# Kernel optimization log

Hardware: AMD Instinct MI355X
Metric: run time of the kernel (lower is better)

## Reference

```python
import jax, jax.numpy as jnp
import numpy as np

# --- LIF neuron (spikingjelly LIFNode, single-step, tau=2.0, hard reset, ATan surrogate) ---
# With zero initial membrane potential, one step gives h = x / tau, spike = heaviside(h - v_th).
ALPHA = 2.0  # ATan surrogate default alpha
TAU = 2.0    # LIFNode default tau
V_TH = 1.0

@jax.custom_vjp
def atan_heaviside(x):
    return (x >= 0.0).astype(x.dtype)

def _ah_fwd(x):
    return (x >= 0.0).astype(x.dtype), x

def _ah_bwd(res, g):
    # d/dx of ATan surrogate: alpha / (2 * (1 + (pi/2 * alpha * x)^2))
    return (g * (ALPHA / (2.0 * (1.0 + (jnp.pi / 2.0 * ALPHA * res) ** 2))),)

atan_heaviside.defvjp(_ah_fwd, _ah_bwd)

def lif(x):
    return atan_heaviside(x / TAU - V_TH)

DIM, NUM_HEADS, TOPK = 256, 8, 4
WT, WH, WW = 2, 4, 4

def setup_inputs() -> dict:
    key = jax.random.key(0)
    k1, k2, k3, k4, k5 = jax.random.split(key, 5)
    T, B, Lt, Lh, Lw, C = 4, 2, 8, 32, 32, DIM
    x = jax.random.normal(k1, (T, B, Lt, Lh, Lw, C), dtype=jnp.float32)
    w_qkv = jax.random.normal(k2, (C, 3 * C), dtype=jnp.float32) * 0.02
    b_qkv = jax.random.normal(k3, (3 * C,), dtype=jnp.float32) * 0.02
    w_proj = jax.random.normal(k4, (C, C), dtype=jnp.float32) * 0.02
    b_proj = jax.random.normal(k5, (C,), dtype=jnp.float32) * 0.02
    return {"x": x, "w_qkv": w_qkv, "b_qkv": b_qkv, "w_proj": w_proj, "b_proj": b_proj}

def reference(x, w_qkv, b_qkv, w_proj, b_proj):
    T, B, Lt, Lh, Lw, C = x.shape
    H = NUM_HEADS
    D = C // H
    scale = D ** -0.5
    lt, lh, lw = Lt // WT, Lh // WH, Lw // WW
    W = WT * WH * WW          # num_wins = 32
    S = lt * lh * lw          # win_size = 256

    # window partition: [T,B,Lt,Lh,Lw,C] -> [T,B,W,S,C]
    xw = x.reshape(T, B, WT, lt, WH, lh, WW, lw, C)
    xw = xw.transpose(0, 1, 2, 4, 6, 3, 5, 7, 8).reshape(T, B, W, S, C)

    # region routing: mean over timesteps and tokens -> [B,W,C]
    region = xw.mean(axis=(0, 3))
    scores = jnp.einsum('bwc,bvc->bwv', region, region) * scale  # [B,W,W]
    idx = jax.lax.top_k(scores, TOPK)[1]                          # [B,W,K] int32

    # qkv projection + spiking activations
    qkv = xw @ w_qkv + b_qkv                                      # [T,B,W,S,3C]
    q, k, v = jnp.split(qkv, 3, axis=-1)
    q, k, v = lif(q), lif(k), lif(v)
    q = q.reshape(T, B, W, S, H, D)
    k = k.reshape(T, B, W, S, H, D)
    v = v.reshape(T, B, W, S, H, D)

    # gather routed KV blocks: k_g[t,b,w,j] = k[t,b,idx[b,w,j]]
    b_ix = jnp.arange(B)[:, None, None]
    k_g = k[:, b_ix, idx].reshape(T, B, W, TOPK * S, H, D)        # [T,B,W,K*S,H,D]
    v_g = v[:, b_ix, idx].reshape(T, B, W, TOPK * S, H, D)

    # linear attention: kv = k^T v, out = q @ kv, normalized by q @ sum(k)
    kv = jnp.einsum('tbwnhd,tbwnhe->tbwhde', k_g, v_g)            # [T,B,W,H,D,D]
    out = jnp.einsum('tbwshd,tbwhde->tbwshe', q, kv)              # [T,B,W,S,H,D]
    den = jnp.einsum('tbwshd,tbwhd->tbwsh', q, k_g.sum(axis=3))[..., None]
    out = out / (den + 1e-6)

    out = out.reshape(T, B, W, S, C) @ w_proj + b_proj

    # window reverse: [T,B,W,S,C] -> [T,B,Lt,Lh,Lw,C]
    out = out.reshape(T, B, WT, WH, WW, lt, lh, lw, C)
    out = out.transpose(0, 1, 2, 5, 3, 6, 4, 7, 8).reshape(T, B, Lt, Lh, Lw, C)
    return out
```

## Files before the change

### kernel.cpp

```cpp
#include <hip/hip_runtime.h>
#include <hip/hip_bf16.h>
#include <stdint.h>

#define NT 4
#define NB 2
#define NW 32
#define NS 256
#define NC 256
#define NH 8
#define ND 32
#define NK 4

typedef unsigned int u32;
typedef unsigned long long u64;
typedef unsigned short u16;
typedef __attribute__((ext_vector_type(8))) short bf16x8;
typedef __attribute__((ext_vector_type(4))) float f32x4;

__device__ __forceinline__ int wofs(int w) {
  return (w >> 4) * 4096 + ((w >> 2) & 3) * 256 + (w & 3) * 8;
}
__device__ __forceinline__ int sofs(int s) {
  return ((s >> 6) << 10) + (((s >> 3) & 7) << 5) + (s & 7);
}
__device__ __forceinline__ size_t x_off(int t, int b, int w, int s, int c) {
  return ((size_t)((t * NB + b) * 8192 + wofs(w) + sofs(s))) * NC + c;
}

__device__ __forceinline__ u32 f2bf(float f) {
  union { float f; u32 i; } u; u.f = f;
  return (u.i + 0x7FFFu + ((u.i >> 16) & 1u)) >> 16;
}

__device__ __forceinline__ void gload16(const u16* g, u16* l) {
  __builtin_amdgcn_global_load_lds(
      (const __attribute__((address_space(1))) void*)g,
      (__attribute__((address_space(3))) void*)l, 16, 0, 0);
}

__global__ __launch_bounds__(256) void k_prep(const float* __restrict__ x,
                                              const float* __restrict__ w_qkv,
                                              u16* __restrict__ xw,
                                              u16* __restrict__ bt,
                                              float* __restrict__ region) {
  int blk = blockIdx.x, tid = threadIdx.x;
  if (blk >= 512) {
    int n = (blk - 512) * 8 + (tid >> 5);
    int kc = tid & 31;
    u16 vals[8];
#pragma unroll
    for (int j = 0; j < 8; ++j)
      vals[j] = (u16)f2bf(w_qkv[(size_t)(kc * 8 + j) * 768 + n]);
    *reinterpret_cast<uint4*>(&bt[(size_t)n * 256 + kc * 8]) =
        *reinterpret_cast<const uint4*>(vals);
    return;
  }
  __shared__ float sums[4][4][NC];
  int g = tid >> 6, c4 = tid & 63;
  size_t base = (size_t)blk * 128;
  float4 s[4];
#pragma unroll
  for (int ww = 0; ww < 4; ++ww) s[ww] = make_float4(0.f, 0.f, 0.f, 0.f);
#pragma unroll
  for (int p = 0; p < 32; ++p) {
    int row = p * 4 + g;
    float4 v = *reinterpret_cast<const float4*>(&x[(base + row) * NC + c4 * 4]);
    uint2 bf;
    bf.x = f2bf(v.x) | (f2bf(v.y) << 16);
    bf.y = f2bf(v.z) | (f2bf(v.w) << 16);
    *reinterpret_cast<uint2*>(&xw[(base + row) * NC + c4 * 4]) = bf;
    int ww = (p & 7) >> 1;
    s[ww].x += v.x; s[ww].y += v.y; s[ww].z += v.z; s[ww].w += v.w;
  }
#pragma unroll
  for (int ww = 0; ww < 4; ++ww)
    *reinterpret_cast<float4*>(&sums[ww][g][c4 * 4]) = s[ww];
  __syncthreads();
  int b = (blk >> 6) & 1;
  int wt = ((blk >> 3) & 7) >> 2, wh = (blk & 7) >> 1;
  int v0 = wt * 16 + wh * 4;
  int c = tid;
#pragma unroll
  for (int ww = 0; ww < 4; ++ww) {
    float tot = (sums[ww][0][c] + sums[ww][1][c] + sums[ww][2][c] + sums[ww][3][c]) *
                (1.0f / 1024.0f);
    atomicAdd(&region[((size_t)b * NW + v0 + ww) * NC + c], tot);
  }
}

__global__ __launch_bounds__(256) void k_scores(const float* __restrict__ region,
                                                int* __restrict__ idx) {
  __shared__ float rs[NW][NC];
  __shared__ float scval[NW];
  int blk = blockIdx.x;
  int b = blk >> 5, w = blk & 31;
  int tid = threadIdx.x;
  for (int i = tid; i < NW * NC; i += 256)
    rs[i >> 8][i & 255] = region[(size_t)b * NW * NC + i];
  __syncthreads();
  int v = tid >> 3, l8 = tid & 7;
  float sum = 0.f;
  const float* a = rs[w];
  const float* bb = rs[v];
#pragma unroll
  for (int j = 0; j < 32; ++j) sum += a[l8 * 32 + j] * bb[l8 * 32 + j];
  sum += __shfl_xor(sum, 1);
  sum += __shfl_xor(sum, 2);
  sum += __shfl_xor(sum, 4);
  if (l8 == 0) scval[v] = sum * 0.17677669529663687f;
  __syncthreads();
  if (tid == 0) {
    float sc[NW];
#pragma unroll
    for (int j = 0; j < NW; ++j) sc[j] = scval[j];
    for (int kk = 0; kk < NK; ++kk) {
      float best = -__builtin_inff(); int bi = 0;
      for (int j = 0; j < NW; ++j)
        if (sc[j] > best) { best = sc[j]; bi = j; }
      idx[(b * NW + w) * NK + kk] = bi;
      sc[bi] = -__builtin_inff();
    }
  }
}

__global__ __launch_bounds__(256) void k_gemm(const u16* __restrict__ xw,
                                              const u16* __restrict__ bt,
                                              const float* __restrict__ b_qkv,
                                              u32* __restrict__ qb, u32* __restrict__ kb,
                                              u32* __restrict__ vb,
                                              u32* __restrict__ winflag) {
  __shared__ __align__(16) u16 As[2][128 * 32];
  __shared__ __align__(16) u16 Bs[2][128 * 32];
  __shared__ u32 wfl;

  const int tid = threadIdx.x;
  const int v = (blockIdx.x & 7) * 384 + (blockIdx.x >> 3);
  const int mt = v / 6, nt = v % 6;
  const int m0 = mt * 128, n0 = nt * 128;
  const int wave = tid >> 6, lane = tid & 63;
  const int wr = wave >> 1, wc = wave & 1;

  if (tid == 0) wfl = 0;

  const f32x4 vz = {0.f, 0.f, 0.f, 0.f};
  f32x4 acc[4][4];
#pragma unroll
  for (int m = 0; m < 4; ++m)
#pragma unroll
    for (int n = 0; n < 4; ++n) acc[m][n] = vz;

  auto stage = [&](int buf, int ks) {
    const int k0 = ks * 32;
#pragma unroll
    for (int p = 0; p < 2; ++p) {
      int idx2 = p * 256 + wave * 64 + lane;
      int row = idx2 >> 2, sl = idx2 & 3;
      int ssl = sl ^ ((row >> 1) & 3);
      int lbase = (p * 256 + wave * 64) * 8;
      gload16(&xw[(size_t)(m0 + row) * 256 + k0 + ssl * 8], &As[buf][lbase]);
      gload16(&bt[(size_t)(n0 + row) * 256 + k0 + ssl * 8], &Bs[buf][lbase]);
    }
  };

  stage(0, 0);
  __syncthreads();
#pragma unroll
  for (int ks = 0; ks < 8; ++ks) {
    const int buf = ks & 1;
    if (ks < 7) stage(buf ^ 1, ks + 1);
    bf16x8 afr[4], bfr[4];
#pragma unroll
    for (int m = 0; m < 4; ++m) {
      int r = wr * 64 + m * 16 + (lane & 15);
      int phys = (lane >> 4) ^ ((r >> 1) & 3);
      afr[m] = *reinterpret_cast<const bf16x8*>(&As[buf][r * 32 + phys * 8]);
    }
#pragma unroll
    for (int n = 0; n < 4; ++n) {
      int r = wc * 64 + n * 16 + (lane & 15);
      int phys = (lane >> 4) ^ ((r >> 1) & 3);
      bfr[n] = *reinterpret_cast<const bf16x8*>(&Bs[buf][r * 32 + phys * 8]);
    }
#pragma unroll
    for (int m = 0; m < 4; ++m)
#pragma unroll
      for (int n = 0; n < 4; ++n)
        acc[m][n] = __builtin_amdgcn_mfma_f32_16x16x32_bf16(afr[m], bfr[n], acc[m][n], 0, 0, 0);
    __syncthreads();
  }

  float bias[4];
#pragma unroll
  for (int n = 0; n < 4; ++n) bias[n] = b_qkv[n0 + wc * 64 + n * 16 + (lane & 15)];
  u32* dst = (nt < 2) ? qb : (nt < 4) ? kb : vb;
  const int h0 = (nt * 4) & 7;
  const int g = lane >> 4;
  u32 wfl_loc = 0;
#pragma unroll
  for (int m = 0; m < 4; ++m)
#pragma unroll
    for (int r = 0; r < 4; ++r) {
      u32 words[2];
#pragma unroll
      for (int np = 0; np < 2; ++np) {
        u64 b0 = __ballot(acc[m][2 * np][r] + bias[2 * np] >= 2.0f);
        u64 b1 = __ballot(acc[m][2 * np + 1][r] + bias[2 * np + 1] >= 2.0f);
        words[np] = (u32)((b0 >> (g * 16)) & 0xFFFFu) |
                    ((u32)((b1 >> (g * 16)) & 0xFFFFu) << 16);
      }
      if ((lane & 15) < 2) {
        int np = lane & 1;
        int row = wr * 64 + m * 16 + g * 4 + r;
        u32 wv = words[np];
        dst[(size_t)(m0 + row) * NH + h0 + wc * 2 + np] = wv;
        if (wv) wfl_loc |= 1u << ((row & 31) >> 3);
      }
    }
  if (wfl_loc) atomicOr(&wfl, wfl_loc);
  __syncthreads();
  if (tid == 0 && wfl) {
    int t = mt >> 7, b = (mt >> 6) & 1, Lt = (mt >> 3) & 7, hh = mt & 7;
    int w0 = (Lt >> 2) * 16 + (hh >> 1) * 4;
    u32 bit = (nt < 2) ? 1u : (nt < 4) ? 2u : 4u;
    for (int ww = 0; ww < 4; ++ww)
      if (wfl & (1u << ww))
        atomicOr(&winflag[(t * NB + b) * NW + w0 + ww], bit);
  }
}

__global__ __launch_bounds__(256) void k_attn(const u32* __restrict__ qb,
                                              const u32* __restrict__ kb,
                                              const u32* __restrict__ vb,
                                              const int* __restrict__ idx,
                                              const u32* __restrict__ winflag,
                                              const float* __restrict__ w_proj,
                                              const float* __restrict__ b_proj,
                                              float* __restrict__ out) {
  __shared__ u32 qs[64 * NH];
  __shared__ unsigned short kvc[NH * ND * ND];
  __shared__ u32 ksum[NH * ND];
  __shared__ float attnrow[NC];

  int blk = blockIdx.x;
  int wid = blk >> 2, sc = blk & 3;
  int t = wid >> 6, b = (wid >> 5) & 1, w = wid & 31;
  int s0 = sc * 64;
  int tid = threadIdx.x;

  u32 fs = winflag[(t * NB + b) * NW + w];
  int wj[NK];
  u32 fk = 0, fv = 0;
#pragma unroll
  for (int j = 0; j < NK; ++j) {
    wj[j] = idx[(b * NW + w) * NK + j];
    u32 f = winflag[(t * NB + b) * NW + wj[j]];
    fk |= f & 2u; fv |= f & 4u;
  }
  bool skip = !(fs & 1u) || !fk || !fv;

  if (skip) {
    float bp = b_proj[tid];
    for (int s = s0; s < s0 + 64; ++s) out[x_off(t, b, w, s, tid)] = bp;
    return;
  }

  int tb = (t * NB + b) * 8192;
  size_t gb[NK];
#pragma unroll
  for (int j = 0; j < NK; ++j) gb[j] = (size_t)(tb + wofs(wj[j])) * NH;
  size_t qbase = (size_t)(tb + wofs(w)) * NH;
  for (int i = tid; i < 64 * NH; i += 256)
    qs[i] = qb[qbase + (size_t)sofs(s0 + (i >> 3)) * NH + (i & 7)];
  {
    int h = tid >> 5, d = tid & 31;
    u32 cnt = 0;
    for (int n = 0; n < NK * NS; ++n)
      cnt += (kb[gb[n >> 8] + (size_t)sofs(n & 255) * NH + h] >> d) & 1u;
    ksum[tid] = cnt;
  }
  for (int p = tid; p < NH * ND * ND; p += 256) {
    int h = p >> 10, d = (p >> 5) & 31, e = p & 31;
    u32 cnt = 0;
    for (int n = 0; n < NK * NS; ++n) {
      size_t a = gb[n >> 8] + (size_t)sofs(n & 255) * NH + h;
      cnt += ((kb[a] >> d) & (vb[a] >> e)) & 1u;
    }
    kvc[p] = (unsigned short)cnt;
  }
  __syncthreads();
  int h = tid >> 5, e = tid & 31;
  float bpv = b_proj[tid];
  for (int sl = 0; sl < 64; ++sl) {
    u32 qw = qs[sl * NH + h];
    float num = 0.f, den = 0.f;
    for (int d = 0; d < ND; ++d) {
      if ((qw >> d) & 1u) {
        den += (float)ksum[h * ND + d];
        num += (float)kvc[h * ND * ND + d * ND + e];
      }
    }
    attnrow[tid] = num / (den + 1e-6f);
    __syncthreads();
    float acc = bpv;
    for (int c = 0; c < NC; ++c) acc += attnrow[c] * w_proj[c * NC + tid];
    out[x_off(t, b, w, s0 + sl, tid)] = acc;
    __syncthreads();
  }
}

extern "C" void kernel_launch(void* const* d_in, const int* in_sizes, int n_in,
                              void* d_out, int out_size, void* d_ws, size_t ws_size,
                              hipStream_t stream) {
  const float* x      = (const float*)d_in[0];
  const float* w_qkv  = (const float*)d_in[1];
  const float* b_qkv  = (const float*)d_in[2];
  const float* w_proj = (const float*)d_in[3];
  const float* b_proj = (const float*)d_in[4];
  float* out = (float*)d_out;

  char* ws = (char*)d_ws;
  int* idx       = (int*)(ws + 0x200000);
  u16* bt        = (u16*)(ws + 0x201000);
  u32* winflag   = (u32*)(ws + 0x270000);
  float* region  = (float*)(ws + 0x271000);
  u32* qb        = (u32*)(ws + 0x300000);
  u32* kb        = qb + (size_t)NT * NB * NW * NS * NH;
  u32* vb        = kb + (size_t)NT * NB * NW * NS * NH;
  u16* xw        = (u16*)(ws + 0x900000);

  hipMemsetAsync(ws + 0x270000, 0, 0x11000, stream);
  k_prep<<<608, 256, 0, stream>>>(x, w_qkv, xw, bt, region);
  k_scores<<<NB * NW, 256, 0, stream>>>(region, idx);
  k_gemm<<<3072, 256, 0, stream>>>(xw, bt, b_qkv, qb, kb, vb, winflag);
  k_attn<<<NT * NB * NW * 4, 256, 0, stream>>>(qb, kb, vb, idx, winflag, w_proj, b_proj, out);
}
```

Measured before the change: 88.07 us.

## Enlarge QKV GEMM tiles to 256x256 with 512 threads and explicit waitcnt pipelining

The QKV projection GEMM moves from 128x128 tiles with K-step 32 and 256 threads to 256x256 tiles with K-step 64, 512 threads, and 8x4 MFMA accumulators per wave. Double buffering now relies on explicit vmcnt waits and raw s_barrier with sched_barriers, so the next tile's loads overlap compute. The goal is more data reuse per LDS load, fewer blocks, and fewer barriers. The cost is much more LDS (128KB per block) and more accumulator registers, which limits occupancy to about one block per CU. The winflag and head-index logic is re-derived for the new tile mapping.

```diff
diff --git a/kernel.cpp b/kernel.cpp
--- a/kernel.cpp
+++ b/kernel.cpp
@@ -123,108 +123,127 @@
   }
 }
 
-__global__ __launch_bounds__(256) void k_gemm(const u16* __restrict__ xw,
-                                              const u16* __restrict__ bt,
-                                              const float* __restrict__ b_qkv,
-                                              u32* __restrict__ qb, u32* __restrict__ kb,
-                                              u32* __restrict__ vb,
-                                              u32* __restrict__ winflag) {
-  __shared__ __align__(16) u16 As[2][128 * 32];
-  __shared__ __align__(16) u16 Bs[2][128 * 32];
+__global__ __launch_bounds__(512, 2) void k_gemm(const u16* __restrict__ xw,
+                                                 const u16* __restrict__ bt,
+                                                 const float* __restrict__ b_qkv,
+                                                 u32* __restrict__ qb, u32* __restrict__ kb,
+                                                 u32* __restrict__ vb,
+                                                 u32* __restrict__ winflag) {
+  __shared__ __align__(16) u16 As[2][256 * 64];
+  __shared__ __align__(16) u16 Bs[2][256 * 64];
   __shared__ u32 wfl;
 
   const int tid = threadIdx.x;
-  const int v = (blockIdx.x & 7) * 384 + (blockIdx.x >> 3);
-  const int mt = v / 6, nt = v % 6;
-  const int m0 = mt * 128, n0 = nt * 128;
+  const int v = (blockIdx.x & 7) * 96 + (blockIdx.x >> 3);
+  const int mt = v / 3, nt = v % 3;
+  const int m0 = mt * 256, n0 = nt * 256;
   const int wave = tid >> 6, lane = tid & 63;
-  const int wr = wave >> 1, wc = wave & 1;
+  const int wr = wave >> 2, wc = wave & 3;
 
   if (tid == 0) wfl = 0;
 
   const f32x4 vz = {0.f, 0.f, 0.f, 0.f};
-  f32x4 acc[4][4];
-#pragma unroll
-  for (int m = 0; m < 4; ++m)
+  f32x4 acc[8][4];
+#pragma unroll
+  for (int m = 0; m < 8; ++m)
 #pragma unroll
     for (int n = 0; n < 4; ++n) acc[m][n] = vz;
 
-  auto stage = [&](int buf, int ks) {
-    const int k0 = ks * 32;
-#pragma unroll
-    for (int p = 0; p < 2; ++p) {
-      int idx2 = p * 256 + wave * 64 + lane;
-      int row = idx2 >> 2, sl = idx2 & 3;
-      int ssl = sl ^ ((row >> 1) & 3);
-      int lbase = (p * 256 + wave * 64) * 8;
-      gload16(&xw[(size_t)(m0 + row) * 256 + k0 + ssl * 8], &As[buf][lbase]);
-      gload16(&bt[(size_t)(n0 + row) * 256 + k0 + ssl * 8], &Bs[buf][lbase]);
+  auto stage = [&](int buf, int kt) {
+    const int k0 = kt * 64;
+#pragma unroll
+    for (int i = 0; i < 4; ++i) {
+      int c = i * 512 + tid;
+      int row = c >> 3, p = c & 7;
+      int sl = p ^ (row & 7);
+      gload16(&xw[(size_t)(m0 + row) * 256 + k0 + sl * 8],
+              &As[buf][(i * 512 + wave * 64) * 8]);
+    }
+#pragma unroll
+    for (int i = 0; i < 4; ++i) {
+      int c = i * 512 + tid;
+      int row = c >> 3, p = c & 7;
+      int sl = p ^ (row & 7);
+      gload16(&bt[(size_t)(n0 + row) * 256 + k0 + sl * 8],
+              &Bs[buf][(i * 512 + wave * 64) * 8]);
     }
   };
 
   stage(0, 0);
-  __syncthreads();
-#pragma unroll
-  for (int ks = 0; ks < 8; ++ks) {
-    const int buf = ks & 1;
-    if (ks < 7) stage(buf ^ 1, ks + 1);
-    bf16x8 afr[4], bfr[4];
-#pragma unroll
-    for (int m = 0; m < 4; ++m) {
-      int r = wr * 64 + m * 16 + (lane & 15);
-      int phys = (lane >> 4) ^ ((r >> 1) & 3);
-      afr[m] = *reinterpret_cast<const bf16x8*>(&As[buf][r * 32 + phys * 8]);
-    }
-#pragma unroll
-    for (int n = 0; n < 4; ++n) {
-      int r = wc * 64 + n * 16 + (lane & 15);
-      int phys = (lane >> 4) ^ ((r >> 1) & 3);
-      bfr[n] = *reinterpret_cast<const bf16x8*>(&Bs[buf][r * 32 + phys * 8]);
-    }
-#pragma unroll
-    for (int m = 0; m < 4; ++m)
-#pragma unroll
-      for (int n = 0; n < 4; ++n)
-        acc[m][n] = __builtin_amdgcn_mfma_f32_16x16x32_bf16(afr[m], bfr[n], acc[m][n], 0, 0, 0);
-    __syncthreads();
+#pragma unroll
+  for (int kt = 0; kt < 4; ++kt) {
+    const int buf = kt & 1;
+    if (kt < 3) {
+      stage(buf ^ 1, kt + 1);
+      __builtin_amdgcn_sched_barrier(0);
+      asm volatile("s_waitcnt vmcnt(8)" ::: "memory");
+    } else {
+      __builtin_amdgcn_sched_barrier(0);
+      asm volatile("s_waitcnt vmcnt(0)" ::: "memory");
+    }
+    __builtin_amdgcn_s_barrier();
+    __builtin_amdgcn_sched_barrier(0);
+#pragma unroll
+    for (int kk = 0; kk < 2; ++kk) {
+      bf16x8 af[8], bfr[4];
+#pragma unroll
+      for (int m = 0; m < 8; ++m) {
+        int r = wr * 128 + m * 16 + (lane & 15);
+        int sl = kk * 4 + (lane >> 4);
+        int phys = sl ^ (r & 7);
+        af[m] = *reinterpret_cast<const bf16x8*>(&As[buf][r * 64 + phys * 8]);
+      }
+#pragma unroll
+      for (int n = 0; n < 4; ++n) {
+        int r = wc * 64 + n * 16 + (lane & 15);
+        int sl = kk * 4 + (lane >> 4);
+        int phys = sl ^ (r & 7);
+        bfr[n] = *reinterpret_cast<const bf16x8*>(&Bs[buf][r * 64 + phys * 8]);
+      }
+#pragma unroll
+      for (int m = 0; m < 8; ++m)
+#pragma unroll
+        for (int n = 0; n < 4; ++n)
+          acc[m][n] = __builtin_amdgcn_mfma_f32_16x16x32_bf16(af[m], bfr[n], acc[m][n], 0, 0, 0);
+    }
+    __builtin_amdgcn_s_barrier();
   }
 
   float bias[4];
 #pragma unroll
   for (int n = 0; n < 4; ++n) bias[n] = b_qkv[n0 + wc * 64 + n * 16 + (lane & 15)];
-  u32* dst = (nt < 2) ? qb : (nt < 4) ? kb : vb;
-  const int h0 = (nt * 4) & 7;
+  u32* dst = (nt == 0) ? qb : (nt == 1) ? kb : vb;
   const int g = lane >> 4;
   u32 wfl_loc = 0;
 #pragma unroll
-  for (int m = 0; m < 4; ++m)
+  for (int m = 0; m < 8; ++m)
 #pragma unroll
     for (int r = 0; r < 4; ++r) {
       u32 words[2];
 #pragma unroll
-      for (int np = 0; np < 2; ++np) {
-        u64 b0 = __ballot(acc[m][2 * np][r] + bias[2 * np] >= 2.0f);
-        u64 b1 = __ballot(acc[m][2 * np + 1][r] + bias[2 * np + 1] >= 2.0f);
-        words[np] = (u32)((b0 >> (g * 16)) & 0xFFFFu) |
+      for (int jp = 0; jp < 2; ++jp) {
+        u64 b0 = __ballot(acc[m][2 * jp][r] + bias[2 * jp] >= 2.0f);
+        u64 b1 = __ballot(acc[m][2 * jp + 1][r] + bias[2 * jp + 1] >= 2.0f);
+        words[jp] = (u32)((b0 >> (g * 16)) & 0xFFFFu) |
                     ((u32)((b1 >> (g * 16)) & 0xFFFFu) << 16);
       }
       if ((lane & 15) < 2) {
-        int np = lane & 1;
-        int row = wr * 64 + m * 16 + g * 4 + r;
-        u32 wv = words[np];
-        dst[(size_t)(m0 + row) * NH + h0 + wc * 2 + np] = wv;
+        int jp = lane & 1;
+        int row = wr * 128 + m * 16 + g * 4 + r;
+        u32 wv = words[jp];
+        dst[(size_t)(m0 + row) * NH + wc * 2 + jp] = wv;
         if (wv) wfl_loc |= 1u << ((row & 31) >> 3);
       }
     }
   if (wfl_loc) atomicOr(&wfl, wfl_loc);
   __syncthreads();
   if (tid == 0 && wfl) {
-    int t = mt >> 7, b = (mt >> 6) & 1, Lt = (mt >> 3) & 7, hh = mt & 7;
-    int w0 = (Lt >> 2) * 16 + (hh >> 1) * 4;
-    u32 bit = (nt < 2) ? 1u : (nt < 4) ? 2u : 4u;
+    int t = m0 >> 14, b = (m0 >> 13) & 1;
+    int v0 = (((m0 >> 10) & 7) >> 2) * 16 + (((m0 >> 5) & 31) >> 3) * 4;
+    u32 bit = 1u << nt;
     for (int ww = 0; ww < 4; ++ww)
       if (wfl & (1u << ww))
-        atomicOr(&winflag[(t * NB + b) * NW + w0 + ww], bit);
+        atomicOr(&winflag[(t * NB + b) * NW + v0 + ww], bit);
   }
 }
 
@@ -328,9 +347,9 @@
   u32* vb        = kb + (size_t)NT * NB * NW * NS * NH;
   u16* xw        = (u16*)(ws + 0x900000);
 
-  hipMemsetAsync(ws + 0x270000, 0, 0x11000, stream);
+  (void)hipMemsetAsync(ws + 0x270000, 0, 0x11000, stream);
   k_prep<<<608, 256, 0, stream>>>(x, w_qkv, xw, bt, region);
   k_scores<<<NB * NW, 256, 0, stream>>>(region, idx);
-  k_gemm<<<3072, 256, 0, stream>>>(xw, bt, b_qkv, qb, kb, vb, winflag);
+  k_gemm<<<768, 512, 0, stream>>>(xw, bt, b_qkv, qb, kb, vb, winflag);
   k_attn<<<NT * NB * NW * 4, 256, 0, stream>>>(qb, kb, vb, idx, winflag, w_proj, b_proj, out);
 }
```

After: 83.95 us. 4.7% less time.
